# Kernel optimization log

Measured on AMD Instinct MI355X. Metric: run time of the kernel, lower is better.

## Reference

```python
import math
import jax, jax.numpy as jnp
import numpy as np

EMBED_DIM = 1024
NUM_HEADS = 16
HEAD_DIM = EMBED_DIM // NUM_HEADS


def setup_inputs() -> dict:
    key = jax.random.key(0)
    ks = jax.random.split(key, 10)
    B, S, E = 2, 2048, EMBED_DIM
    x = jax.random.normal(ks[0], (B, S, E), dtype=jnp.float32)
    mask = jax.random.randint(ks[1], (B, S), 0, 2, dtype=jnp.int32)
    s = 1.0 / math.sqrt(E)
    Wq = jax.random.normal(ks[2], (E, E), dtype=jnp.float32) * s
    bq = jnp.zeros((E,), dtype=jnp.float32)
    Wk = jax.random.normal(ks[3], (E, E), dtype=jnp.float32) * s
    bk = jnp.zeros((E,), dtype=jnp.float32)
    Wv = jax.random.normal(ks[4], (E, E), dtype=jnp.float32) * s
    bv = jnp.zeros((E,), dtype=jnp.float32)
    Wo = jax.random.normal(ks[5], (E, E), dtype=jnp.float32) * s
    bo = jnp.zeros((E,), dtype=jnp.float32)
    return {"x": x, "mask": mask, "Wq": Wq, "bq": bq, "Wk": Wk, "bk": bk,
            "Wv": Wv, "bv": bv, "Wo": Wo, "bo": bo}


def reference(x, mask, Wq, bq, Wk, bk, Wv, bv, Wo, bo):
    B, S, E = x.shape
    H, D = NUM_HEADS, HEAD_DIM
    scale = math.sqrt(D)  # ScaledDotProductAttention built with head_dim

    def split_heads(t):
        return t.reshape(B, S, H, D).transpose(0, 2, 1, 3)  # [B,H,S,D]

    q = split_heads(x @ Wq + bq)
    k = split_heads(x @ Wk + bk)
    v = split_heads(x @ Wv + bv)

    scores = jnp.einsum('bhqd,bhkd->bhqk', q, k) / scale  # [B,H,S,S]
    m = mask[:, None, None, :].astype(scores.dtype)        # [B,1,1,S]
    neg = jnp.finfo(scores.dtype).min
    scores = jnp.where(m == 0, neg, scores)
    aw = jax.nn.softmax(scores, axis=-1)
    # post-softmax mask renormalization (as in the torch module)
    aw = aw * m
    denom = aw.sum(axis=-1, keepdims=True)
    aw = jnp.where(denom > 0, aw / jnp.where(denom > 0, denom, 1.0), 0.0)

    ctx = jnp.einsum('bhqk,bhkd->bhqd', aw, v)             # [B,H,S,D]
    ctx = ctx.transpose(0, 2, 1, 3).reshape(B, S, E)
    out = ctx @ Wo + bo
    return out
```

## Files before the change

### kernel.cpp

```cpp
#include <hip/hip_runtime.h>

typedef _Float16 half8 __attribute__((ext_vector_type(8)));
typedef _Float16 half4v __attribute__((ext_vector_type(4)));
typedef _Float16 h2 __attribute__((ext_vector_type(2)));
typedef float f4 __attribute__((ext_vector_type(4)));

#define ASYNC_COPY16(ldsp, gp)                                                     \
  __builtin_amdgcn_global_load_lds((__attribute__((address_space(1))) void*)(gp),  \
                                   (__attribute__((address_space(3))) void*)(ldsp),\
                                   16, 0, 0)

__device__ __forceinline__ f4 mfma16(half8 a, half8 b, f4 c) {
  return __builtin_amdgcn_mfma_f32_16x16x32_f16(a, b, c, 0, 0, 0);
}

__device__ __forceinline__ h2 pack2(float a, float b) {
  return __builtin_bit_cast(h2, __builtin_amdgcn_cvt_pkrtz(a, b));
}

#if defined(__has_builtin)
#if __has_builtin(__builtin_amdgcn_exp2f)
#define EXP2(x) __builtin_amdgcn_exp2f(x)
#endif
#endif
#ifndef EXP2
#define EXP2(x) __expf((x) * 0.69314718056f)
#endif
#define KSCALE 0.18033688011f
#define FIXMAX 10.0f


__global__ __launch_bounds__(256) void k_prep(
    const float* __restrict__ x, _Float16* __restrict__ xh,
    const float* __restrict__ Wq, const float* __restrict__ Wk,
    const float* __restrict__ Wv, const float* __restrict__ Wo,
    _Float16* __restrict__ wqkvT, _Float16* __restrict__ woT) {
  __shared__ float tw[32][33];
  const int bid = blockIdx.x, t = threadIdx.x;
  if (bid < 4096) {
    int i = (bid * 256 + t) * 4;
    f4 v = *(const f4*)(x + i);
    half4v h;
    h[0] = (_Float16)v[0]; h[1] = (_Float16)v[1];
    h[2] = (_Float16)v[2]; h[3] = (_Float16)v[3];
    *(half4v*)(xh + i) = h;
    return;
  }
  const int idx = bid - 4096;
  const int z = idx >> 10, rem = idx & 1023;
  const int n0 = (rem & 31) * 32, k0 = (rem >> 5) * 32;
  const float* w = (z == 0) ? Wq : (z == 1) ? Wk : (z == 2) ? Wv : Wo;
  _Float16* wt = (z == 3) ? woT : wqkvT + (size_t)z * 1048576;
  const int tx = t & 31, ty = t >> 5;
  for (int j = 0; j < 32; j += 8) tw[ty + j][tx] = w[(size_t)(k0 + ty + j) * 1024 + n0 + tx];
  __syncthreads();
  for (int j = 0; j < 32; j += 8)
    wt[(size_t)(n0 + ty + j) * 1024 + k0 + tx] = (_Float16)tw[tx][ty + j];
}

__global__ __launch_bounds__(256) void k_gemm_proj(
    const _Float16* __restrict__ A, const _Float16* __restrict__ Bt,
    const float* __restrict__ bq, const float* __restrict__ bk, const float* __restrict__ bv,
    _Float16* __restrict__ Qo, _Float16* __restrict__ Ko, _Float16* __restrict__ Vto) {
  __shared__ __align__(16) _Float16 As[128 * 64];
  __shared__ __align__(16) _Float16 Bs[128 * 64];
  const int t = threadIdx.x, lane = t & 63, w = t >> 6;
  const int qd = lane >> 4, lr = lane & 15;
  const int m0 = blockIdx.y * 128, n0 = blockIdx.x * 128;
  const int wm = (w & 1) * 64, wn = (w >> 1) * 64;
  const f4 z4 = {0.f, 0.f, 0.f, 0.f};
  f4 acc[4][4];
#pragma unroll
  for (int i = 0; i < 4; ++i)
#pragma unroll
    for (int j = 0; j < 4; ++j) acc[i][j] = z4;

  const int sr = t >> 3;
  const int sc8 = (t & 7) * 8;
  for (int k0 = 0; k0 < 1024; k0 += 64) {
#pragma unroll
    for (int c = 0; c < 4; ++c) {
      const _Float16* ga = A + (size_t)(m0 + c * 32 + sr) * 1024 + k0 + sc8;
      const _Float16* gb = Bt + (size_t)(n0 + c * 32 + sr) * 1024 + k0 + sc8;
      ASYNC_COPY16((char*)As + c * 4096 + w * 1024, ga);
      ASYNC_COPY16((char*)Bs + c * 4096 + w * 1024, gb);
    }
    __syncthreads();
#pragma unroll
    for (int ks = 0; ks < 2; ++ks) {
      half8 af[4], bf[4];
#pragma unroll
      for (int i = 0; i < 4; ++i)
        af[i] = *(const half8*)(As + (wm + i * 16 + lr) * 64 + ks * 32 + qd * 8);
#pragma unroll
      for (int j = 0; j < 4; ++j)
        bf[j] = *(const half8*)(Bs + (wn + j * 16 + lr) * 64 + ks * 32 + qd * 8);
#pragma unroll
      for (int i = 0; i < 4; ++i)
#pragma unroll
        for (int j = 0; j < 4; ++j) acc[i][j] = mfma16(af[i], bf[j], acc[i][j]);
    }
    __syncthreads();
  }

  const int mat = n0 >> 10;
  const float* bias = (mat == 0) ? bq : (mat == 1) ? bk : bv;
  if (mat == 2) {
#pragma unroll
    for (int i = 0; i < 4; ++i)
#pragma unroll
      for (int j = 0; j < 4; ++j) {
        int n = (n0 + wn + j * 16 + lr) & 1023;
        int hh = n >> 6, d = n & 63;
        int mb = m0 + wm + i * 16 + qd * 4;
        int bb = mb >> 11, sb = mb & 2047;
        float bval = bias[n];
        half4v hv;
#pragma unroll
        for (int r = 0; r < 4; ++r) hv[r] = (_Float16)(acc[i][j][r] + bval);
        *(half4v*)(Vto + ((size_t)(bb * 16 + hh) * 64 + d) * 2048 + sb) = hv;
      }
  } else {
    _Float16* outp = (mat == 0) ? Qo : Ko;
    const float scl = (mat == 0) ? KSCALE : 1.f;
#pragma unroll
    for (int i = 0; i < 4; ++i)
#pragma unroll
      for (int j = 0; j < 4; ++j)
#pragma unroll
        for (int r = 0; r < 4; ++r) {
          int m = m0 + wm + i * 16 + qd * 4 + r;
          int n = (n0 + wn + j * 16 + lr) & 1023;
          float v = (acc[i][j][r] + bias[n]) * scl;
          int bb = m >> 11, s = m & 2047, hh = n >> 6, d = n & 63;
          outp[(size_t)((bb * 16 + hh) * 2048 + s) * 64 + d] = (_Float16)v;
        }
  }
}

__global__ __launch_bounds__(256, 2) void k_attn(
    const _Float16* __restrict__ Qg, const _Float16* __restrict__ Kg,
    const _Float16* __restrict__ Vtg, const int* __restrict__ maskg,
    _Float16* __restrict__ Op, float* __restrict__ ml) {
  __shared__ __align__(16) _Float16 Ks[64][72];
  __shared__ __align__(16) _Float16 Vts[64][72];
  __shared__ __align__(16) _Float16 Pq[4][16][72];
  __shared__ float Msk[64];

  const int bh = blockIdx.y;
  const int b = bh >> 4;
  const int q0 = blockIdx.x * 256;
  const int z = blockIdx.z;
  const int kb = z * 1024;
  const int t = threadIdx.x, lane = t & 63, w = t >> 6;
  const int qd = lane >> 4, lr = lane & 15;

  half8 qf[4][2];
#pragma unroll
  for (int rt = 0; rt < 4; ++rt)
#pragma unroll
    for (int ks = 0; ks < 2; ++ks)
      qf[rt][ks] = *(const half8*)(Qg + (size_t)(bh * 2048 + q0 + w * 64 + rt * 16 + lr) * 64 +
                                   ks * 32 + qd * 8);

  const f4 z4 = {0.f, 0.f, 0.f, 0.f};
  f4 O[4][4];
  f4 Ol[4];
#pragma unroll
  for (int rt = 0; rt < 4; ++rt) {
    Ol[rt] = z4;
#pragma unroll
    for (int dt = 0; dt < 4; ++dt) O[rt][dt] = z4;
  }
  half8 ones8;
#pragma unroll
  for (int j = 0; j < 8; ++j) ones8[j] = (_Float16)1.f;

  const int sr0 = t >> 3, scc = (t & 7) * 8;
  const int sr1 = sr0 + 32;
  const _Float16* Kbase = Kg + (size_t)bh * 2048 * 64 + (size_t)kb * 64;
  const _Float16* Vtbase = Vtg + (size_t)bh * 64 * 2048 + kb;

  f4 kr0 = *(const f4*)(Kbase + (size_t)sr0 * 64 + scc);
  f4 kr1 = *(const f4*)(Kbase + (size_t)sr1 * 64 + scc);
  f4 vr0 = *(const f4*)(Vtbase + (size_t)sr0 * 2048 + scc);
  f4 vr1 = *(const f4*)(Vtbase + (size_t)sr1 * 2048 + scc);
  float mval = 0.f;
  if (t < 64) mval = maskg[b * 2048 + kb + t] ? -FIXMAX : -30010.f;

  for (int it = 0; it < 16; ++it) {
    __syncthreads();
    *(f4*)&Ks[sr0][scc] = kr0;
    *(f4*)&Ks[sr1][scc] = kr1;
    *(f4*)&Vts[sr0][scc] = vr0;
    *(f4*)&Vts[sr1][scc] = vr1;
    if (t < 64) Msk[t] = mval;
    __syncthreads();

    if (it < 15) {
      int kk = (it + 1) * 64;
      kr0 = *(const f4*)(Kbase + (size_t)(kk + sr0) * 64 + scc);
      kr1 = *(const f4*)(Kbase + (size_t)(kk + sr1) * 64 + scc);
      vr0 = *(const f4*)(Vtbase + (size_t)sr0 * 2048 + kk + scc);
      vr1 = *(const f4*)(Vtbase + (size_t)sr1 * 2048 + kk + scc);
      if (t < 64) mval = maskg[b * 2048 + kb + kk + t] ? -FIXMAX : -30010.f;
    }

    half8 kf0[4], kf1[4];
#pragma unroll
    for (int kt = 0; kt < 4; ++kt) {
      kf0[kt] = *(const half8*)&Ks[kt * 16 + lr][qd * 8];
      kf1[kt] = *(const half8*)&Ks[kt * 16 + lr][32 + qd * 8];
    }

    half8 bp[4][2];
#pragma unroll
    for (int rtp = 0; rtp < 2; ++rtp) {
      const int r0 = rtp * 2, r1 = rtp * 2 + 1;
      f4 sc[2][4];
#pragma unroll
      for (int kt = 0; kt < 4; ++kt) {
        f4 mv = *(const f4*)&Msk[kt * 16 + qd * 4];
        sc[0][kt] = mv;
        sc[1][kt] = mv;
      }
      __builtin_amdgcn_s_setprio(1);
#pragma unroll
      for (int kt = 0; kt < 4; ++kt) {
        sc[0][kt] = mfma16(kf0[kt], qf[r0][0], sc[0][kt]);
        sc[0][kt] = mfma16(kf1[kt], qf[r0][1], sc[0][kt]);
        sc[1][kt] = mfma16(kf0[kt], qf[r1][0], sc[1][kt]);
        sc[1][kt] = mfma16(kf1[kt], qf[r1][1], sc[1][kt]);
      }
      __builtin_amdgcn_s_setprio(0);

#pragma unroll
      for (int rr = 0; rr < 2; ++rr) {
        const int rt = rtp * 2 + rr;
#pragma unroll
        for (int kt = 0; kt < 4; ++kt) {
          float p0 = EXP2(sc[rr][kt][0]);
          float p1 = EXP2(sc[rr][kt][1]);
          float p2 = EXP2(sc[rr][kt][2]);
          float p3 = EXP2(sc[rr][kt][3]);
          half4v hv;
          hv.lo = pack2(p0, p1);
          hv.hi = pack2(p2, p3);
          *(half4v*)&Pq[w][lr][kt * 16 + qd * 4] = hv;
        }
        bp[rt][0] = *(const half8*)&Pq[w][lr][qd * 8];
        bp[rt][1] = *(const half8*)&Pq[w][lr][32 + qd * 8];
      }
    }

    __builtin_amdgcn_s_setprio(1);
#pragma unroll
    for (int dt = 0; dt < 4; ++dt) {
      half8 va0 = *(const half8*)&Vts[dt * 16 + lr][qd * 8];
      half8 va1 = *(const half8*)&Vts[dt * 16 + lr][32 + qd * 8];
#pragma unroll
      for (int rt = 0; rt < 4; ++rt) {
        O[rt][dt] = mfma16(va0, bp[rt][0], O[rt][dt]);
        O[rt][dt] = mfma16(va1, bp[rt][1], O[rt][dt]);
      }
    }
#pragma unroll
    for (int rt = 0; rt < 4; ++rt) {
      Ol[rt] = mfma16(ones8, bp[rt][0], Ol[rt]);
      Ol[rt] = mfma16(ones8, bp[rt][1], Ol[rt]);
    }
    __builtin_amdgcn_s_setprio(0);
  }

#pragma unroll
  for (int rt = 0; rt < 4; ++rt) {
    int qrow = q0 + w * 64 + rt * 16 + lr;
    size_t rowi = (size_t)(z * 32 + bh) * 2048 + qrow;
    _Float16* op = Op + rowi * 64;
#pragma unroll
    for (int dt = 0; dt < 4; ++dt) {
      half4v hv;
#pragma unroll
      for (int r = 0; r < 4; ++r) hv[r] = (_Float16)O[rt][dt][r];
      *(half4v*)(op + dt * 16 + qd * 4) = hv;
    }
    if (qd == 0) ml[rowi] = Ol[rt][0];
  }
}

__global__ __launch_bounds__(256) void k_merge(const _Float16* __restrict__ Op,
                                               const float* __restrict__ ml,
                                               _Float16* __restrict__ ctx) {
  int idx = blockIdx.x * 256 + threadIdx.x;
  int d8 = (idx & 7) * 8;
  int h = (idx >> 3) & 15;
  int q = idx >> 7;
  int b = q >> 11, s = q & 2047;
  int bh = b * 16 + h;
  size_t r1 = (size_t)bh * 2048 + s;
  size_t r2 = (size_t)(32 + bh) * 2048 + s;
  float l1 = ml[r1], l2 = ml[r2];
  float inv = 1.f / fmaxf(l1 + l2, 1e-20f);
  half8 o1 = *(const half8*)(Op + r1 * 64 + d8);
  half8 o2 = *(const half8*)(Op + r2 * 64 + d8);
  half8 ho;
#pragma unroll
  for (int j = 0; j < 8; ++j)
    ho[j] = (_Float16)(((float)o1[j] + (float)o2[j]) * inv);
  *(half8*)(ctx + (size_t)q * 1024 + h * 64 + d8) = ho;
}

__global__ __launch_bounds__(256) void k_gemm_out(
    const _Float16* __restrict__ A, const _Float16* __restrict__ Bt,
    const float* __restrict__ bo, float* __restrict__ out) {
  __shared__ __align__(16) _Float16 As[64 * 32];
  __shared__ __align__(16) _Float16 Bs[128 * 32];
  const int t = threadIdx.x, lane = t & 63, w = t >> 6;
  const int qd = lane >> 4, lr = lane & 15;
  const int m0 = blockIdx.y * 64, n0 = blockIdx.x * 128;
  const int wm = (w & 1) * 32, wn = (w >> 1) * 64;
  const f4 z4 = {0.f, 0.f, 0.f, 0.f};
  f4 acc[2][4];
#pragma unroll
  for (int i = 0; i < 2; ++i)
#pragma unroll
    for (int j = 0; j < 4; ++j) acc[i][j] = z4;

  const int c0 = t, c1 = t + 256;
  for (int k0 = 0; k0 < 1024; k0 += 32) {
    const _Float16* ga = A + (size_t)(m0 + (t >> 2)) * 1024 + k0 + (t & 3) * 8;
    const _Float16* gb0 = Bt + (size_t)(n0 + (c0 >> 2)) * 1024 + k0 + (c0 & 3) * 8;
    const _Float16* gb1 = Bt + (size_t)(n0 + (c1 >> 2)) * 1024 + k0 + (c1 & 3) * 8;
    char* la = (char*)As + w * 1024;
    char* lb = (char*)Bs + w * 1024;
    ASYNC_COPY16(la, ga);
    ASYNC_COPY16(lb, gb0);
    ASYNC_COPY16(lb + 4096, gb1);
    __syncthreads();
    half8 af[2], bf[4];
#pragma unroll
    for (int i = 0; i < 2; ++i)
      af[i] = *(const half8*)(As + (wm + i * 16 + lr) * 32 + qd * 8);
#pragma unroll
    for (int j = 0; j < 4; ++j)
      bf[j] = *(const half8*)(Bs + (wn + j * 16 + lr) * 32 + qd * 8);
#pragma unroll
    for (int i = 0; i < 2; ++i)
#pragma unroll
      for (int j = 0; j < 4; ++j) acc[i][j] = mfma16(af[i], bf[j], acc[i][j]);
    __syncthreads();
  }
#pragma unroll
  for (int i = 0; i < 2; ++i)
#pragma unroll
    for (int j = 0; j < 4; ++j)
#pragma unroll
      for (int r = 0; r < 4; ++r) {
        int m = m0 + wm + i * 16 + qd * 4 + r;
        int n = n0 + wn + j * 16 + lr;
        out[(size_t)m * 1024 + n] = acc[i][j][r] + bo[n];
      }
}

extern "C" void kernel_launch(void* const* d_in, const int* in_sizes, int n_in,
                              void* d_out, int out_size, void* d_ws, size_t ws_size,
                              hipStream_t stream) {
  const float* x = (const float*)d_in[0];
  const int* mask = (const int*)d_in[1];
  const float* Wq = (const float*)d_in[2];
  const float* bq = (const float*)d_in[3];
  const float* Wk = (const float*)d_in[4];
  const float* bk = (const float*)d_in[5];
  const float* Wv = (const float*)d_in[6];
  const float* bv = (const float*)d_in[7];
  const float* Wo = (const float*)d_in[8];
  const float* bo = (const float*)d_in[9];
  float* out = (float*)d_out;
  char* ws = (char*)d_ws;
  const size_t MB = 1 << 20;

  _Float16* Oph   = (_Float16*)(ws + 0);
  _Float16* xh    = (_Float16*)(ws + 0);
  _Float16* wqkvT = (_Float16*)(ws + 8 * MB);
  _Float16* woT   = (_Float16*)(ws + 16 * MB);
  _Float16* Qh    = (_Float16*)(ws + 18 * MB);
  _Float16* ctxh  = (_Float16*)(ws + 18 * MB);
  _Float16* Kh    = (_Float16*)(ws + 26 * MB);
  _Float16* Vth   = (_Float16*)(ws + 34 * MB);
  float*    mlw   = (float*)   (ws + 42 * MB);

  k_prep<<<dim3(8192), dim3(256), 0, stream>>>(x, xh, Wq, Wk, Wv, Wo, wqkvT, woT);
  k_gemm_proj<<<dim3(24, 32), dim3(256), 0, stream>>>(xh, wqkvT, bq, bk, bv, Qh, Kh, Vth);
  k_attn<<<dim3(8, 32, 2), dim3(256), 0, stream>>>(Qh, Kh, Vth, mask, Oph, mlw);
  k_merge<<<dim3(2048), dim3(256), 0, stream>>>(Oph, mlw, ctxh);
  k_gemm_out<<<dim3(8, 64), dim3(256), 0, stream>>>(ctxh, woT, bo, out);
}
```

Baseline: 213.5 us.

## Fuse split-KV merge into output projection GEMM and shrink proj K-tile

Removes the separate k_merge kernel: the output GEMM now reads both split-KV partial outputs and their softmax sums, normalizes them, and writes the A tile into LDS directly. This saves one launch and a full write and read of the context tensor. The merge work is recomputed by each of the 8 column blocks, and the A loads become synchronous. Separately, the QKV projection GEMM's K-step drops from 64 to 32, halving LDS use at the cost of twice as many barriers.

```diff
diff --git a/kernel.cpp b/kernel.cpp
--- a/kernel.cpp
+++ b/kernel.cpp
@@ -62,8 +62,8 @@
     const _Float16* __restrict__ A, const _Float16* __restrict__ Bt,
     const float* __restrict__ bq, const float* __restrict__ bk, const float* __restrict__ bv,
     _Float16* __restrict__ Qo, _Float16* __restrict__ Ko, _Float16* __restrict__ Vto) {
-  __shared__ __align__(16) _Float16 As[128 * 64];
-  __shared__ __align__(16) _Float16 Bs[128 * 64];
+  __shared__ __align__(16) _Float16 As[128 * 32];
+  __shared__ __align__(16) _Float16 Bs[128 * 32];
   const int t = threadIdx.x, lane = t & 63, w = t >> 6;
   const int qd = lane >> 4, lr = lane & 15;
   const int m0 = blockIdx.y * 128, n0 = blockIdx.x * 128;
@@ -75,31 +75,30 @@
 #pragma unroll
     for (int j = 0; j < 4; ++j) acc[i][j] = z4;
 
-  const int sr = t >> 3;
-  const int sc8 = (t & 7) * 8;
-  for (int k0 = 0; k0 < 1024; k0 += 64) {
-#pragma unroll
-    for (int c = 0; c < 4; ++c) {
-      const _Float16* ga = A + (size_t)(m0 + c * 32 + sr) * 1024 + k0 + sc8;
-      const _Float16* gb = Bt + (size_t)(n0 + c * 32 + sr) * 1024 + k0 + sc8;
-      ASYNC_COPY16((char*)As + c * 4096 + w * 1024, ga);
-      ASYNC_COPY16((char*)Bs + c * 4096 + w * 1024, gb);
-    }
-    __syncthreads();
-#pragma unroll
-    for (int ks = 0; ks < 2; ++ks) {
-      half8 af[4], bf[4];
-#pragma unroll
-      for (int i = 0; i < 4; ++i)
-        af[i] = *(const half8*)(As + (wm + i * 16 + lr) * 64 + ks * 32 + qd * 8);
-#pragma unroll
-      for (int j = 0; j < 4; ++j)
-        bf[j] = *(const half8*)(Bs + (wn + j * 16 + lr) * 64 + ks * 32 + qd * 8);
-#pragma unroll
-      for (int i = 0; i < 4; ++i)
-#pragma unroll
-        for (int j = 0; j < 4; ++j) acc[i][j] = mfma16(af[i], bf[j], acc[i][j]);
-    }
+  const int c0 = t, c1 = t + 256;
+  for (int k0 = 0; k0 < 1024; k0 += 32) {
+    const _Float16* ga0 = A + (size_t)(m0 + (c0 >> 2)) * 1024 + k0 + (c0 & 3) * 8;
+    const _Float16* ga1 = A + (size_t)(m0 + (c1 >> 2)) * 1024 + k0 + (c1 & 3) * 8;
+    const _Float16* gb0 = Bt + (size_t)(n0 + (c0 >> 2)) * 1024 + k0 + (c0 & 3) * 8;
+    const _Float16* gb1 = Bt + (size_t)(n0 + (c1 >> 2)) * 1024 + k0 + (c1 & 3) * 8;
+    char* la = (char*)As + w * 1024;
+    char* lb = (char*)Bs + w * 1024;
+    ASYNC_COPY16(la, ga0);
+    ASYNC_COPY16(la + 4096, ga1);
+    ASYNC_COPY16(lb, gb0);
+    ASYNC_COPY16(lb + 4096, gb1);
+    __syncthreads();
+    half8 af[4], bf[4];
+#pragma unroll
+    for (int i = 0; i < 4; ++i)
+      af[i] = *(const half8*)(As + (wm + i * 16 + lr) * 32 + qd * 8);
+#pragma unroll
+    for (int j = 0; j < 4; ++j)
+      bf[j] = *(const half8*)(Bs + (wn + j * 16 + lr) * 32 + qd * 8);
+#pragma unroll
+    for (int i = 0; i < 4; ++i)
+#pragma unroll
+      for (int j = 0; j < 4; ++j) acc[i][j] = mfma16(af[i], bf[j], acc[i][j]);
     __syncthreads();
   }
 
@@ -288,30 +287,9 @@
   }
 }
 
-__global__ __launch_bounds__(256) void k_merge(const _Float16* __restrict__ Op,
-                                               const float* __restrict__ ml,
-                                               _Float16* __restrict__ ctx) {
-  int idx = blockIdx.x * 256 + threadIdx.x;
-  int d8 = (idx & 7) * 8;
-  int h = (idx >> 3) & 15;
-  int q = idx >> 7;
-  int b = q >> 11, s = q & 2047;
-  int bh = b * 16 + h;
-  size_t r1 = (size_t)bh * 2048 + s;
-  size_t r2 = (size_t)(32 + bh) * 2048 + s;
-  float l1 = ml[r1], l2 = ml[r2];
-  float inv = 1.f / fmaxf(l1 + l2, 1e-20f);
-  half8 o1 = *(const half8*)(Op + r1 * 64 + d8);
-  half8 o2 = *(const half8*)(Op + r2 * 64 + d8);
-  half8 ho;
-#pragma unroll
-  for (int j = 0; j < 8; ++j)
-    ho[j] = (_Float16)(((float)o1[j] + (float)o2[j]) * inv);
-  *(half8*)(ctx + (size_t)q * 1024 + h * 64 + d8) = ho;
-}
-
 __global__ __launch_bounds__(256) void k_gemm_out(
-    const _Float16* __restrict__ A, const _Float16* __restrict__ Bt,
+    const _Float16* __restrict__ Op, const float* __restrict__ ml,
+    const _Float16* __restrict__ Bt,
     const float* __restrict__ bo, float* __restrict__ out) {
   __shared__ __align__(16) _Float16 As[64 * 32];
   __shared__ __align__(16) _Float16 Bs[128 * 32];
@@ -326,14 +304,28 @@
 #pragma unroll
     for (int j = 0; j < 4; ++j) acc[i][j] = z4;
 
+  const int ar = t >> 2, ac8 = (t & 3) * 8;
+  const int m = m0 + ar;
+  const int b = m >> 11, s = m & 2047;
+
   const int c0 = t, c1 = t + 256;
   for (int k0 = 0; k0 < 1024; k0 += 32) {
-    const _Float16* ga = A + (size_t)(m0 + (t >> 2)) * 1024 + k0 + (t & 3) * 8;
+    const int h = k0 >> 6;
+    const int d0 = (k0 & 63) + ac8;
+    const size_t r1 = (size_t)(b * 16 + h) * 2048 + s;
+    const size_t r2 = r1 + (size_t)32 * 2048;
+    const float inv = 1.f / fmaxf(ml[r1] + ml[r2], 1e-20f);
+    half8 o1 = *(const half8*)(Op + r1 * 64 + d0);
+    half8 o2 = *(const half8*)(Op + r2 * 64 + d0);
+    half8 ha;
+#pragma unroll
+    for (int j = 0; j < 8; ++j)
+      ha[j] = (_Float16)(((float)o1[j] + (float)o2[j]) * inv);
+    *(half8*)(As + ar * 32 + ac8) = ha;
+
     const _Float16* gb0 = Bt + (size_t)(n0 + (c0 >> 2)) * 1024 + k0 + (c0 & 3) * 8;
     const _Float16* gb1 = Bt + (size_t)(n0 + (c1 >> 2)) * 1024 + k0 + (c1 & 3) * 8;
-    char* la = (char*)As + w * 1024;
     char* lb = (char*)Bs + w * 1024;
-    ASYNC_COPY16(la, ga);
     ASYNC_COPY16(lb, gb0);
     ASYNC_COPY16(lb + 4096, gb1);
     __syncthreads();
@@ -356,9 +348,9 @@
     for (int j = 0; j < 4; ++j)
 #pragma unroll
       for (int r = 0; r < 4; ++r) {
-        int m = m0 + wm + i * 16 + qd * 4 + r;
+        int mm = m0 + wm + i * 16 + qd * 4 + r;
         int n = n0 + wn + j * 16 + lr;
-        out[(size_t)m * 1024 + n] = acc[i][j][r] + bo[n];
+        out[(size_t)mm * 1024 + n] = acc[i][j][r] + bo[n];
       }
 }
 
@@ -384,7 +376,6 @@
   _Float16* wqkvT = (_Float16*)(ws + 8 * MB);
   _Float16* woT   = (_Float16*)(ws + 16 * MB);
   _Float16* Qh    = (_Float16*)(ws + 18 * MB);
-  _Float16* ctxh  = (_Float16*)(ws + 18 * MB);
   _Float16* Kh    = (_Float16*)(ws + 26 * MB);
   _Float16* Vth   = (_Float16*)(ws + 34 * MB);
   float*    mlw   = (float*)   (ws + 42 * MB);
@@ -392,6 +383,5 @@
   k_prep<<<dim3(8192), dim3(256), 0, stream>>>(x, xh, Wq, Wk, Wv, Wo, wqkvT, woT);
   k_gemm_proj<<<dim3(24, 32), dim3(256), 0, stream>>>(xh, wqkvT, bq, bk, bv, Qh, Kh, Vth);
   k_attn<<<dim3(8, 32, 2), dim3(256), 0, stream>>>(Qh, Kh, Vth, mask, Oph, mlw);
-  k_merge<<<dim3(2048), dim3(256), 0, stream>>>(Oph, mlw, ctxh);
-  k_gemm_out<<<dim3(8, 64), dim3(256), 0, stream>>>(ctxh, woT, bo, out);
-}
+  k_gemm_out<<<dim3(8, 64), dim3(256), 0, stream>>>(Oph, mlw, woT, bo, out);
+}
```

Measured after the change: 201.2 us. 5.8% less time.

## Double attention K/V tile to 128 keys and shrink projection GEMM k-step

Applied to the files above, without the earlier changes.

The attention kernel now stages 128 keys of K, V and mask per iteration instead of 64. This halves the number of barrier pairs and loop iterations, with the 128-key tile processed as two 64-key halves. The projection GEMM moves from a 64-wide to a 32-wide k-step, which halves its LDS tiles but doubles the number of synchronizations. In exchange, attention uses more registers and LDS for prefetch, which could reduce occupancy, and the GEMM pays more barriers per unit of work.

```diff
diff --git a/kernel.cpp b/kernel.cpp
--- a/kernel.cpp
+++ b/kernel.cpp
@@ -62,8 +62,8 @@
     const _Float16* __restrict__ A, const _Float16* __restrict__ Bt,
     const float* __restrict__ bq, const float* __restrict__ bk, const float* __restrict__ bv,
     _Float16* __restrict__ Qo, _Float16* __restrict__ Ko, _Float16* __restrict__ Vto) {
-  __shared__ __align__(16) _Float16 As[128 * 64];
-  __shared__ __align__(16) _Float16 Bs[128 * 64];
+  __shared__ __align__(16) _Float16 As[128 * 32];
+  __shared__ __align__(16) _Float16 Bs[128 * 32];
   const int t = threadIdx.x, lane = t & 63, w = t >> 6;
   const int qd = lane >> 4, lr = lane & 15;
   const int m0 = blockIdx.y * 128, n0 = blockIdx.x * 128;
@@ -75,31 +75,30 @@
 #pragma unroll
     for (int j = 0; j < 4; ++j) acc[i][j] = z4;
 
-  const int sr = t >> 3;
-  const int sc8 = (t & 7) * 8;
-  for (int k0 = 0; k0 < 1024; k0 += 64) {
-#pragma unroll
-    for (int c = 0; c < 4; ++c) {
-      const _Float16* ga = A + (size_t)(m0 + c * 32 + sr) * 1024 + k0 + sc8;
-      const _Float16* gb = Bt + (size_t)(n0 + c * 32 + sr) * 1024 + k0 + sc8;
-      ASYNC_COPY16((char*)As + c * 4096 + w * 1024, ga);
-      ASYNC_COPY16((char*)Bs + c * 4096 + w * 1024, gb);
-    }
-    __syncthreads();
-#pragma unroll
-    for (int ks = 0; ks < 2; ++ks) {
-      half8 af[4], bf[4];
-#pragma unroll
-      for (int i = 0; i < 4; ++i)
-        af[i] = *(const half8*)(As + (wm + i * 16 + lr) * 64 + ks * 32 + qd * 8);
-#pragma unroll
-      for (int j = 0; j < 4; ++j)
-        bf[j] = *(const half8*)(Bs + (wn + j * 16 + lr) * 64 + ks * 32 + qd * 8);
-#pragma unroll
-      for (int i = 0; i < 4; ++i)
-#pragma unroll
-        for (int j = 0; j < 4; ++j) acc[i][j] = mfma16(af[i], bf[j], acc[i][j]);
-    }
+  const int c0 = t, c1 = t + 256;
+  for (int k0 = 0; k0 < 1024; k0 += 32) {
+    const _Float16* ga0 = A + (size_t)(m0 + (c0 >> 2)) * 1024 + k0 + (c0 & 3) * 8;
+    const _Float16* ga1 = A + (size_t)(m0 + (c1 >> 2)) * 1024 + k0 + (c1 & 3) * 8;
+    const _Float16* gb0 = Bt + (size_t)(n0 + (c0 >> 2)) * 1024 + k0 + (c0 & 3) * 8;
+    const _Float16* gb1 = Bt + (size_t)(n0 + (c1 >> 2)) * 1024 + k0 + (c1 & 3) * 8;
+    char* la = (char*)As + w * 1024;
+    char* lb = (char*)Bs + w * 1024;
+    ASYNC_COPY16(la, ga0);
+    ASYNC_COPY16(la + 4096, ga1);
+    ASYNC_COPY16(lb, gb0);
+    ASYNC_COPY16(lb + 4096, gb1);
+    __syncthreads();
+    half8 af[4], bf[4];
+#pragma unroll
+    for (int i = 0; i < 4; ++i)
+      af[i] = *(const half8*)(As + (wm + i * 16 + lr) * 32 + qd * 8);
+#pragma unroll
+    for (int j = 0; j < 4; ++j)
+      bf[j] = *(const half8*)(Bs + (wn + j * 16 + lr) * 32 + qd * 8);
+#pragma unroll
+    for (int i = 0; i < 4; ++i)
+#pragma unroll
+      for (int j = 0; j < 4; ++j) acc[i][j] = mfma16(af[i], bf[j], acc[i][j]);
     __syncthreads();
   }
 
@@ -142,10 +141,10 @@
     const _Float16* __restrict__ Qg, const _Float16* __restrict__ Kg,
     const _Float16* __restrict__ Vtg, const int* __restrict__ maskg,
     _Float16* __restrict__ Op, float* __restrict__ ml) {
-  __shared__ __align__(16) _Float16 Ks[64][72];
-  __shared__ __align__(16) _Float16 Vts[64][72];
+  __shared__ __align__(16) _Float16 Ks[128][72];
+  __shared__ __align__(16) _Float16 Vts[64][136];
   __shared__ __align__(16) _Float16 Pq[4][16][72];
-  __shared__ float Msk[64];
+  __shared__ float Msk[128];
 
   const int bh = blockIdx.y;
   const int b = bh >> 4;
@@ -176,100 +175,109 @@
 #pragma unroll
   for (int j = 0; j < 8; ++j) ones8[j] = (_Float16)1.f;
 
-  const int sr0 = t >> 3, scc = (t & 7) * 8;
-  const int sr1 = sr0 + 32;
+  const int ksr = t >> 3, ksc = (t & 7) * 8;
+  const int vsr = t >> 4, vsc = (t & 15) * 8;
   const _Float16* Kbase = Kg + (size_t)bh * 2048 * 64 + (size_t)kb * 64;
   const _Float16* Vtbase = Vtg + (size_t)bh * 64 * 2048 + kb;
 
-  f4 kr0 = *(const f4*)(Kbase + (size_t)sr0 * 64 + scc);
-  f4 kr1 = *(const f4*)(Kbase + (size_t)sr1 * 64 + scc);
-  f4 vr0 = *(const f4*)(Vtbase + (size_t)sr0 * 2048 + scc);
-  f4 vr1 = *(const f4*)(Vtbase + (size_t)sr1 * 2048 + scc);
+  f4 kr[4], vr[4];
+#pragma unroll
+  for (int i = 0; i < 4; ++i) {
+    kr[i] = *(const f4*)(Kbase + (size_t)(i * 32 + ksr) * 64 + ksc);
+    vr[i] = *(const f4*)(Vtbase + (size_t)(i * 16 + vsr) * 2048 + vsc);
+  }
   float mval = 0.f;
-  if (t < 64) mval = maskg[b * 2048 + kb + t] ? -FIXMAX : -30010.f;
-
-  for (int it = 0; it < 16; ++it) {
-    __syncthreads();
-    *(f4*)&Ks[sr0][scc] = kr0;
-    *(f4*)&Ks[sr1][scc] = kr1;
-    *(f4*)&Vts[sr0][scc] = vr0;
-    *(f4*)&Vts[sr1][scc] = vr1;
-    if (t < 64) Msk[t] = mval;
-    __syncthreads();
-
-    if (it < 15) {
-      int kk = (it + 1) * 64;
-      kr0 = *(const f4*)(Kbase + (size_t)(kk + sr0) * 64 + scc);
-      kr1 = *(const f4*)(Kbase + (size_t)(kk + sr1) * 64 + scc);
-      vr0 = *(const f4*)(Vtbase + (size_t)sr0 * 2048 + kk + scc);
-      vr1 = *(const f4*)(Vtbase + (size_t)sr1 * 2048 + kk + scc);
-      if (t < 64) mval = maskg[b * 2048 + kb + kk + t] ? -FIXMAX : -30010.f;
+  if (t < 128) mval = maskg[b * 2048 + kb + t] ? -FIXMAX : -30010.f;
+
+  for (int it = 0; it < 8; ++it) {
+    __syncthreads();
+#pragma unroll
+    for (int i = 0; i < 4; ++i) {
+      *(f4*)&Ks[i * 32 + ksr][ksc] = kr[i];
+      *(f4*)&Vts[i * 16 + vsr][vsc] = vr[i];
     }
-
-    half8 kf0[4], kf1[4];
-#pragma unroll
-    for (int kt = 0; kt < 4; ++kt) {
-      kf0[kt] = *(const half8*)&Ks[kt * 16 + lr][qd * 8];
-      kf1[kt] = *(const half8*)&Ks[kt * 16 + lr][32 + qd * 8];
+    if (t < 128) Msk[t] = mval;
+    __syncthreads();
+
+    if (it < 7) {
+      int kk = (it + 1) * 128;
+#pragma unroll
+      for (int i = 0; i < 4; ++i) {
+        kr[i] = *(const f4*)(Kbase + (size_t)(kk + i * 32 + ksr) * 64 + ksc);
+        vr[i] = *(const f4*)(Vtbase + (size_t)(i * 16 + vsr) * 2048 + kk + vsc);
+      }
+      if (t < 128) mval = maskg[b * 2048 + kb + kk + t] ? -FIXMAX : -30010.f;
     }
 
-    half8 bp[4][2];
-#pragma unroll
-    for (int rtp = 0; rtp < 2; ++rtp) {
-      const int r0 = rtp * 2, r1 = rtp * 2 + 1;
-      f4 sc[2][4];
+#pragma unroll
+    for (int half = 0; half < 2; ++half) {
+      const int hb = half * 64;
+
+      half8 kf0[4], kf1[4];
 #pragma unroll
       for (int kt = 0; kt < 4; ++kt) {
-        f4 mv = *(const f4*)&Msk[kt * 16 + qd * 4];
-        sc[0][kt] = mv;
-        sc[1][kt] = mv;
-      }
+        kf0[kt] = *(const half8*)&Ks[hb + kt * 16 + lr][qd * 8];
+        kf1[kt] = *(const half8*)&Ks[hb + kt * 16 + lr][32 + qd * 8];
+      }
+
+      half8 bp[4][2];
+#pragma unroll
+      for (int rtp = 0; rtp < 2; ++rtp) {
+        const int r0 = rtp * 2, r1 = rtp * 2 + 1;
+        f4 sc[2][4];
+#pragma unroll
+        for (int kt = 0; kt < 4; ++kt) {
+          f4 mv = *(const f4*)&Msk[hb + kt * 16 + qd * 4];
+          sc[0][kt] = mv;
+          sc[1][kt] = mv;
+        }
+        __builtin_amdgcn_s_setprio(1);
+#pragma unroll
+        for (int kt = 0; kt < 4; ++kt) {
+          sc[0][kt] = mfma16(kf0[kt], qf[r0][0], sc[0][kt]);
+          sc[0][kt] = mfma16(kf1[kt], qf[r0][1], sc[0][kt]);
+          sc[1][kt] = mfma16(kf0[kt], qf[r1][0], sc[1][kt]);
+          sc[1][kt] = mfma16(kf1[kt], qf[r1][1], sc[1][kt]);
+        }
+        __builtin_amdgcn_s_setprio(0);
+
+#pragma unroll
+        for (int rr = 0; rr < 2; ++rr) {
+          const int rt = rtp * 2 + rr;
+#pragma unroll
+          for (int kt = 0; kt < 4; ++kt) {
+            float p0 = EXP2(sc[rr][kt][0]);
+            float p1 = EXP2(sc[rr][kt][1]);
+            float p2 = EXP2(sc[rr][kt][2]);
+            float p3 = EXP2(sc[rr][kt][3]);
+            half4v hv;
+            hv.lo = pack2(p0, p1);
+            hv.hi = pack2(p2, p3);
+            *(half4v*)&Pq[w][lr][kt * 16 + qd * 4] = hv;
+          }
+          bp[rt][0] = *(const half8*)&Pq[w][lr][qd * 8];
+          bp[rt][1] = *(const half8*)&Pq[w][lr][32 + qd * 8];
+        }
+      }
+
       __builtin_amdgcn_s_setprio(1);
 #pragma unroll
-      for (int kt = 0; kt < 4; ++kt) {
-        sc[0][kt] = mfma16(kf0[kt], qf[r0][0], sc[0][kt]);
-        sc[0][kt] = mfma16(kf1[kt], qf[r0][1], sc[0][kt]);
-        sc[1][kt] = mfma16(kf0[kt], qf[r1][0], sc[1][kt]);
-        sc[1][kt] = mfma16(kf1[kt], qf[r1][1], sc[1][kt]);
+      for (int dt = 0; dt < 4; ++dt) {
+        half8 va0 = *(const half8*)&Vts[dt * 16 + lr][hb + qd * 8];
+        half8 va1 = *(const half8*)&Vts[dt * 16 + lr][hb + 32 + qd * 8];
+#pragma unroll
+        for (int rt = 0; rt < 4; ++rt) {
+          O[rt][dt] = mfma16(va0, bp[rt][0], O[rt][dt]);
+          O[rt][dt] = mfma16(va1, bp[rt][1], O[rt][dt]);
+        }
+      }
+#pragma unroll
+      for (int rt = 0; rt < 4; ++rt) {
+        Ol[rt] = mfma16(ones8, bp[rt][0], Ol[rt]);
+        Ol[rt] = mfma16(ones8, bp[rt][1], Ol[rt]);
       }
       __builtin_amdgcn_s_setprio(0);
-
-#pragma unroll
-      for (int rr = 0; rr < 2; ++rr) {
-        const int rt = rtp * 2 + rr;
-#pragma unroll
-        for (int kt = 0; kt < 4; ++kt) {
-          float p0 = EXP2(sc[rr][kt][0]);
-          float p1 = EXP2(sc[rr][kt][1]);
-          float p2 = EXP2(sc[rr][kt][2]);
-          float p3 = EXP2(sc[rr][kt][3]);
-          half4v hv;
-          hv.lo = pack2(p0, p1);
-          hv.hi = pack2(p2, p3);
-          *(half4v*)&Pq[w][lr][kt * 16 + qd * 4] = hv;
-        }
-        bp[rt][0] = *(const half8*)&Pq[w][lr][qd * 8];
-        bp[rt][1] = *(const half8*)&Pq[w][lr][32 + qd * 8];
-      }
     }
-
-    __builtin_amdgcn_s_setprio(1);
-#pragma unroll
-    for (int dt = 0; dt < 4; ++dt) {
-      half8 va0 = *(const half8*)&Vts[dt * 16 + lr][qd * 8];
-      half8 va1 = *(const half8*)&Vts[dt * 16 + lr][32 + qd * 8];
-#pragma unroll
-      for (int rt = 0; rt < 4; ++rt) {
-        O[rt][dt] = mfma16(va0, bp[rt][0], O[rt][dt]);
-        O[rt][dt] = mfma16(va1, bp[rt][1], O[rt][dt]);
-      }
-    }
-#pragma unroll
-    for (int rt = 0; rt < 4; ++rt) {
-      Ol[rt] = mfma16(ones8, bp[rt][0], Ol[rt]);
-      Ol[rt] = mfma16(ones8, bp[rt][1], Ol[rt]);
-    }
-    __builtin_amdgcn_s_setprio(0);
   }
 
 #pragma unroll
```

Result: faster. 197.4 us (-7.5%).
